# Optimization experiments

Measured on AMD Instinct MI355X. Metric: run time of the kernel, lower is better.

The kernel has to match this reference:

```python
import jax, jax.numpy as jnp
import numpy as np

# SqueezeSeg CRF config
NUM_CLASS = 4
SIZE_Z, SIZE_A = 3, 5            # LCN_HEIGHT, LCN_WIDTH
B, H, W = 16, 64, 512            # batch, zenith, azimuth
RCRF_ITER = 3
BI_FILTER_COEF = 0.1
ANG_FILTER_COEF = 0.02
ANG_THETA_A = 0.9
BILATERAL_THETA_A = 0.9
K = SIZE_Z * SIZE_A              # 15 -> 14 neighbors (center excluded)

# neighbor offsets of the 3x5 condensing kernel, center excluded
OFFSETS = [(dz, da) for dz in range(SIZE_Z) for da in range(SIZE_A)
           if not (dz == SIZE_Z // 2 and da == SIZE_A // 2)]

def _gauss_weights(theta_sq):
    # angular_filter_kernel: Gaussian of squared spatial offset, center zeroed
    g = [np.exp(-((dz - SIZE_Z // 2) ** 2 + (da - SIZE_A // 2) ** 2) / (2.0 * theta_sq))
         for dz, da in OFFSETS]
    return jnp.asarray(np.array(g, dtype=np.float32))

def gather_neighbors(x):
    # x: [B,C,H,W] -> [B,C,K-1,H,W]; zero-padded 'same' neighborhood gather
    pz, pa = SIZE_Z // 2, SIZE_A // 2
    xp = jnp.pad(x, ((0, 0), (0, 0), (pz, pz), (pa, pa)))
    return jnp.stack([xp[:, :, dz:dz + H, da:da + W] for dz, da in OFFSETS], axis=2)

def setup_inputs() -> dict:
    key = jax.random.key(0)
    k1, k2, k3 = jax.random.split(key, 3)
    x = jax.random.normal(k1, (B, NUM_CLASS, H, W), dtype=jnp.float32)
    bilateral_filters = jax.random.uniform(k2, (B, 1, K - 1, H, W), dtype=jnp.float32)
    lidar_mask = (jax.random.uniform(k3, (B, 1, H, W)) > 0.5).astype(jnp.float32)
    return {"x": x, "bilateral_filters": bilateral_filters, "lidar_mask": lidar_mask}

def reference(x, bilateral_filters, lidar_mask):
    g_ang = _gauss_weights(ANG_THETA_A ** 2)
    g_bi = _gauss_weights(BILATERAL_THETA_A ** 2)
    compat = jnp.ones((NUM_CLASS, NUM_CLASS), jnp.float32) - jnp.eye(NUM_CLASS, dtype=jnp.float32)
    ang_compat = compat * ANG_FILTER_COEF   # [out_class, in_class] 1x1 conv
    bi_compat = compat * BI_FILTER_COEF

    for _ in range(RCRF_ITER):
        unary = jax.nn.softmax(x, axis=1)                     # softmax over class dim
        nb = gather_neighbors(unary)                          # [B,C,14,H,W]
        # depthwise angular filters = Gaussian-weighted neighbor sums
        ang = jnp.einsum('k,bckhw->bchw', g_ang, nb)
        bi_ang = jnp.einsum('k,bckhw->bchw', g_bi, nb)
        # condensing conv on masked unary, weighted by per-pixel bilateral filters
        nb_m = gather_neighbors(unary * lidar_mask)           # [B,C,14,H,W]
        condensed = jnp.sum(nb_m * bilateral_filters, axis=2) # [B,C,H,W]
        bi = condensed * lidar_mask * bi_ang
        # 1x1 compatibility transforms
        ang2 = jnp.einsum('oc,bchw->bohw', ang_compat, ang)
        bi2 = jnp.einsum('oc,bchw->bohw', bi_compat, bi)
        x = unary + ang2 + bi2
    return x
```

## Files before the change

kernel.cpp:

```cpp
#include <hip/hip_runtime.h>


#define NCLASS 4
#define HH 64
#define WW 512
#define BB 16
#define TH 8
#define TW 64
#define UR (TH + 6)
#define UC (TW + 12)
#define PLANE (HH * WW)

#define G1 0.53940412f
#define G2 0.29095687f
#define G4 0.08466190f
#define G5 0.04566227f

#define TAPS                                                                 \
    const int   DZ[14] = {-1,-1,-1,-1,-1,  0, 0, 0, 0,  1, 1, 1, 1, 1};      \
    const int   DA[14] = {-2,-1, 0, 1, 2, -2,-1, 1, 2, -2,-1, 0, 1, 2};      \
    const float GW[14] = {G5,G2,G1,G2,G5, G4,G1,G1,G4, G5,G2,G1,G2,G5};

__device__ __forceinline__ float4 softmax4(float4 v) {
    const float mx = fmaxf(fmaxf(v.x, v.y), fmaxf(v.z, v.w));
    const float e0 = __expf(v.x - mx);
    const float e1 = __expf(v.y - mx);
    const float e2 = __expf(v.z - mx);
    const float e3 = __expf(v.w - mx);
    const float inv = 1.0f / (e0 + e1 + e2 + e3);
    return make_float4(e0 * inv, e1 * inv, e2 * inv, e3 * inv);
}

template <int MR, int MC, bool FINAL>
__device__ __forceinline__ void crf_step(
    const float4 (*__restrict__ u_src)[UC],
    float4 (*__restrict__ u_dst)[UC],
    const float (*__restrict__ m_lds)[UC],
    const float* __restrict__ filt, float* __restrict__ dst,
    int b, int h0, int w0, int tid)
{
    constexpr int RH = TH + 2 * MR;
    constexpr int RW = TW + 2 * MC;
    constexpr int NS = (RH * RW + 255) / 256;
    TAPS

#pragma unroll
    for (int j = 0; j < NS; ++j) {
        const int s = tid + 256 * j;
        if (s < RH * RW) {
            const int lr = s / RW;
            const int lc = s - lr * RW;
            const int gh = h0 + lr - MR;
            const int gw = w0 + lc - MC;
            const int ur = lr + (3 - MR);
            const int uc = lc + (6 - MC);
            const bool in = (gh >= 0) && (gh < HH) && (gw >= 0) && (gw < WW);
            float4 r = make_float4(0.f, 0.f, 0.f, 0.f);
            if (in) {
                float F[14];
                const float* fp = filt + ((size_t)b * 14 * HH + gh) * WW + gw;
#pragma unroll
                for (int k = 0; k < 14; ++k)
                    F[k] = fp[(size_t)k * PLANE];

                float a0 = 0.f, a1 = 0.f, a2 = 0.f, a3 = 0.f;
                float c0 = 0.f, c1 = 0.f, c2 = 0.f, c3 = 0.f;
                const float mcen = m_lds[ur][uc];
#pragma unroll
                for (int k = 0; k < 14; ++k) {
                    const float  mn = m_lds[ur + DZ[k]][uc + DA[k]];
                    const float4 u  = u_src[ur + DZ[k]][uc + DA[k]];
                    const float  fm = F[k] * mn;
                    const float  gk = GW[k];
                    a0 = fmaf(gk, u.x, a0);  c0 = fmaf(fm, u.x, c0);
                    a1 = fmaf(gk, u.y, a1);  c1 = fmaf(fm, u.y, c1);
                    a2 = fmaf(gk, u.z, a2);  c2 = fmaf(fm, u.z, c2);
                    a3 = fmaf(gk, u.w, a3);  c3 = fmaf(fm, u.w, c3);
                }
                const float b0 = c0 * mcen * a0;
                const float b1 = c1 * mcen * a1;
                const float b2 = c2 * mcen * a2;
                const float b3 = c3 * mcen * a3;
                const float sa = a0 + a1 + a2 + a3;
                const float sb = b0 + b1 + b2 + b3;
                const float4 ucen = u_src[ur][uc];
                r.x = ucen.x + 0.02f * (sa - a0) + 0.1f * (sb - b0);
                r.y = ucen.y + 0.02f * (sa - a1) + 0.1f * (sb - b1);
                r.z = ucen.z + 0.02f * (sa - a2) + 0.1f * (sb - b2);
                r.w = ucen.w + 0.02f * (sa - a3) + 0.1f * (sb - b3);
            }
            if (FINAL) {
                if (in) {
                    float* o = dst + ((size_t)b * NCLASS * HH + gh) * WW + gw;
                    o[0]         = r.x;
                    o[PLANE]     = r.y;
                    o[2 * PLANE] = r.z;
                    o[3 * PLANE] = r.w;
                }
            } else {
                u_dst[ur][uc] = in ? softmax4(r)
                                   : make_float4(0.f, 0.f, 0.f, 0.f);
            }
        }
    }
    if (!FINAL) __syncthreads();
}

__global__ __launch_bounds__(256, 4) void crf_fused(
    const float* __restrict__ xin,
    const float* __restrict__ filt,
    const float* __restrict__ mask,
    float* __restrict__ xout)
{
    __shared__ float4 uA[UR][UC];
    __shared__ float4 uB[UR][UC];
    __shared__ float  m_lds[UR][UC];

    const int b   = blockIdx.z;
    const int h0  = blockIdx.y * TH;
    const int w0  = blockIdx.x * TW;
    const int tid = threadIdx.x;

    for (int idx = tid; idx < UR * UC; idx += 256) {
        const int lr = idx / UC;
        const int lc = idx - lr * UC;
        const int gh = h0 + lr - 3;
        const int gw = w0 + lc - 6;
        float4 u = make_float4(0.f, 0.f, 0.f, 0.f);
        float  m = 0.f;
        if (gh >= 0 && gh < HH && gw >= 0 && gw < WW) {
            const float* px = xin + ((size_t)b * NCLASS * HH + gh) * WW + gw;
            u = softmax4(make_float4(px[0], px[PLANE], px[2 * PLANE], px[3 * PLANE]));
            m = mask[((size_t)b * HH + gh) * WW + gw];
        }
        uA[lr][lc]    = u;
        m_lds[lr][lc] = m;
    }
    __syncthreads();

    crf_step<2, 4, false>(uA, uB, m_lds, filt, xout, b, h0, w0, tid);
    crf_step<1, 2, false>(uB, uA, m_lds, filt, xout, b, h0, w0, tid);
    crf_step<0, 0, true >(uA, uB, m_lds, filt, xout, b, h0, w0, tid);
}

extern "C" void kernel_launch(void* const* d_in, const int* in_sizes, int n_in,
                              void* d_out, int out_size, void* d_ws, size_t ws_size,
                              hipStream_t stream) {
    const float* x    = (const float*)d_in[0];
    const float* filt = (const float*)d_in[1];
    const float* msk  = (const float*)d_in[2];
    float* out = (float*)d_out;
    (void)d_ws; (void)ws_size;

    dim3 grid(WW / TW, HH / TH, BB);
    dim3 block(256);
    crf_fused<<<grid, block, 0, stream>>>(x, filt, msk, out);
}
```

Baseline: 100.4 us.

## Precompute softmax into packed float4 buffer and stream filter loads per tap

Adds a separate kernel that computes the initial softmax once per pixel and stores it as an interleaved float4 array in workspace. The fused CRF kernel then loads halo tiles from this buffer with one vector load, so overlapping halos no longer redo the four strided loads and the softmax. The 14 bilateral filter loads are also moved into the accumulation loop instead of being gathered up front, which may lower register pressure at the cost of less load batching. The extra launch and the round trip through the workspace buffer add traffic and latency.

Measured after the change: 101.8 us. No clear change (+1.4%).

```diff
diff --git a/kernel.cpp b/kernel.cpp
--- a/kernel.cpp
+++ b/kernel.cpp
@@ -10,6 +10,7 @@
 #define UR (TH + 6)
 #define UC (TW + 12)
 #define PLANE (HH * WW)
+#define NPIX (BB * HH * WW)
 
 #define G1 0.53940412f
 #define G2 0.29095687f
@@ -29,6 +30,16 @@
     const float e3 = __expf(v.w - mx);
     const float inv = 1.0f / (e0 + e1 + e2 + e3);
     return make_float4(e0 * inv, e1 * inv, e2 * inv, e3 * inv);
+}
+
+__global__ __launch_bounds__(256) void softmax_pack(
+    const float* __restrict__ x, float4* __restrict__ up)
+{
+    const int i = blockIdx.x * 256 + threadIdx.x;
+    const int b = i >> 15;
+    const int p = i & 32767;
+    const float* px = x + (size_t)b * NCLASS * PLANE + p;
+    up[i] = softmax4(make_float4(px[0], px[PLANE], px[2 * PLANE], px[3 * PLANE]));
 }
 
 template <int MR, int MC, bool FINAL>
@@ -57,20 +68,16 @@
             const bool in = (gh >= 0) && (gh < HH) && (gw >= 0) && (gw < WW);
             float4 r = make_float4(0.f, 0.f, 0.f, 0.f);
             if (in) {
-                float F[14];
-                const float* fp = filt + ((size_t)b * 14 * HH + gh) * WW + gw;
-#pragma unroll
-                for (int k = 0; k < 14; ++k)
-                    F[k] = fp[(size_t)k * PLANE];
-
                 float a0 = 0.f, a1 = 0.f, a2 = 0.f, a3 = 0.f;
                 float c0 = 0.f, c1 = 0.f, c2 = 0.f, c3 = 0.f;
                 const float mcen = m_lds[ur][uc];
+                const float* fp = filt + ((size_t)b * 14 * HH + gh) * WW + gw;
 #pragma unroll
                 for (int k = 0; k < 14; ++k) {
+                    const float  f  = fp[(size_t)k * PLANE];
                     const float  mn = m_lds[ur + DZ[k]][uc + DA[k]];
                     const float4 u  = u_src[ur + DZ[k]][uc + DA[k]];
-                    const float  fm = F[k] * mn;
+                    const float  fm = f * mn;
                     const float  gk = GW[k];
                     a0 = fmaf(gk, u.x, a0);  c0 = fmaf(fm, u.x, c0);
                     a1 = fmaf(gk, u.y, a1);  c1 = fmaf(fm, u.y, c1);
@@ -107,7 +114,7 @@
 }
 
 __global__ __launch_bounds__(256, 4) void crf_fused(
-    const float* __restrict__ xin,
+    const float4* __restrict__ u0,
     const float* __restrict__ filt,
     const float* __restrict__ mask,
     float* __restrict__ xout)
@@ -129,9 +136,9 @@
         float4 u = make_float4(0.f, 0.f, 0.f, 0.f);
         float  m = 0.f;
         if (gh >= 0 && gh < HH && gw >= 0 && gw < WW) {
-            const float* px = xin + ((size_t)b * NCLASS * HH + gh) * WW + gw;
-            u = softmax4(make_float4(px[0], px[PLANE], px[2 * PLANE], px[3 * PLANE]));
-            m = mask[((size_t)b * HH + gh) * WW + gw];
+            const int p = ((b * HH) + gh) * WW + gw;
+            u = u0[p];
+            m = mask[p];
         }
         uA[lr][lc]    = u;
         m_lds[lr][lc] = m;
@@ -150,9 +157,11 @@
     const float* filt = (const float*)d_in[1];
     const float* msk  = (const float*)d_in[2];
     float* out = (float*)d_out;
-    (void)d_ws; (void)ws_size;
+    float4* u0 = (float4*)d_ws;
+
+    softmax_pack<<<NPIX / 256, 256, 0, stream>>>(x, u0);
 
     dim3 grid(WW / TW, HH / TH, BB);
     dim3 block(256);
-    crf_fused<<<grid, block, 0, stream>>>(x, filt, msk, out);
+    crf_fused<<<grid, block, 0, stream>>>(u0, filt, msk, out);
 }
```
